# Kernel tuning notes

Hardware: AMD Instinct MI355X
Metric: run time of the kernel (lower is better)

Reference implementation:

```python
import jax, jax.numpy as jnp
import numpy as np

ALPHA = 0.2  # LeakyReLU negative slope
MASK_VAL = -9e15


def gat_layer(h, W, a, adj):
    # h: (b, n, f_in); W: (H, f_in, d); a: (H, 2d, 1); adj: (n, n)
    Wh = jnp.einsum('bni,hid->bhnd', h, W)          # (b, H, n, d)
    d = W.shape[-1]
    a1 = a[:, :d, 0]                                # (H, d) -> source term
    a2 = a[:, d:, 0]                                # (H, d) -> target term
    f1 = jnp.einsum('bhnd,hd->bhn', Wh, a1)
    f2 = jnp.einsum('bhnd,hd->bhn', Wh, a2)
    e = jax.nn.leaky_relu(f1[..., :, None] + f2[..., None, :], ALPHA)  # (b, H, n, n)
    e = jnp.where(adj > 0, e, MASK_VAL)
    att = jax.nn.softmax(e, axis=-1)
    out = jnp.einsum('bhij,bhjd->bhid', att, Wh)    # (b, H, n, d)
    b, H, n, dd = out.shape
    # concat heads along feature dim (matches torch.cat(head_outputs, dim=2))
    return jnp.transpose(out, (0, 2, 1, 3)).reshape(b, n, H * dd)


def setup_inputs() -> dict:
    key = jax.random.key(0)
    ks = jax.random.split(key, 8)
    B, N = 131072, 9
    HID, OUT, HEADS = 96, 48, 3
    hd1 = HID // HEADS   # 32
    hd2 = OUT // HEADS   # 16

    def xavier(k, shape, gain=1.414):
        fan_in, fan_out = shape[-2], shape[-1]
        lim = gain * np.sqrt(6.0 / (fan_in + fan_out))
        return jax.random.uniform(k, shape, jnp.float32, -lim, lim)

    obs = jax.random.normal(ks[0], (B, N), dtype=jnp.float32)
    adj = jnp.ones((N, N), dtype=jnp.float32)
    W1 = xavier(ks[1], (HEADS, 1, hd1))
    a1 = xavier(ks[2], (HEADS, 2 * hd1, 1))
    W2 = xavier(ks[3], (HEADS, HID, hd2))
    a2 = xavier(ks[4], (HEADS, 2 * hd2, 1))
    lim = np.sqrt(1.0 / OUT)
    Wp1 = jax.random.uniform(ks[5], (OUT, OUT // 2), jnp.float32, -lim, lim)
    bp1 = jnp.zeros((OUT // 2,), jnp.float32)
    lim2 = np.sqrt(1.0 / (OUT // 2))
    Wp2 = jax.random.uniform(ks[6], (OUT // 2, 1), jnp.float32, -lim2, lim2)
    bp2 = jnp.zeros((1,), jnp.float32)
    return {"obs": obs, "adj": adj, "W1": W1, "a1": a1, "W2": W2, "a2": a2,
            "Wp1": Wp1, "bp1": bp1, "Wp2": Wp2, "bp2": bp2}


def reference(obs, adj, W1, a1, W2, a2, Wp1, bp1, Wp2, bp2):
    h = obs[..., None]                       # (b, n, 1)
    h = jax.nn.elu(gat_layer(h, W1, a1, adj))
    h = gat_layer(h, W2, a2, adj)            # (b, n, output_dim)
    # attention pooling over nodes
    scores = jnp.tanh(h @ Wp1 + bp1) @ Wp2 + bp2   # (b, n, 1)
    w = jax.nn.softmax(scores, axis=1)
    return jnp.sum(w * h, axis=1)            # (b, output_dim)
```

## Files before the change

### kernel.cpp

```cpp
#include <hip/hip_runtime.h>
#include <math.h>

typedef _Float16 h16;
typedef _Float16 v2h __attribute__((ext_vector_type(2)));

#define ALPHA 0.2f
#define MASKV -9000000000000000.0f

constexpr int GSCR = 268;
constexpr int O_S  = 0;
constexpr int O_F1 = 28;
constexpr int O_F2 = 56;
constexpr int O_U  = 92;

#if defined(__has_builtin)
#  if __has_builtin(__builtin_amdgcn_fdot2)
#    define FDOT2(a,b,c) __builtin_amdgcn_fdot2((a),(b),(c),false)
#  endif
#endif
#ifndef FDOT2
__device__ __forceinline__ float fdot2_sw(v2h a, v2h b, float c) {
    return c + (float)a.x*(float)b.x + (float)a.y*(float)b.y;
}
#  define FDOT2(a,b,c) fdot2_sw((a),(b),(c))
#endif

union U4 { float4 f; v2h h[4]; };
union U2 { float2 f; v2h h[2]; };
union U1 { float  f; v2h h;    };

#define WAVE_SYNC() asm volatile("s_waitcnt lgkmcnt(0)" ::: "memory")

__device__ __forceinline__ float fast_rcp(float x) { return __builtin_amdgcn_rcpf(x); }
__device__ __forceinline__ float tanh_fast(float x) {
    float e = __expf(x + x);
    return 1.f - 2.f * fast_rcp(e + 1.f);
}

__global__ void prep_kernel(const float* __restrict__ W2, const float* __restrict__ Wp1,
                            h16* __restrict__ ws) {
    int t = blockIdx.x * 256 + threadIdx.x;
    if (t < 48 * 96) {
        int c = t / 96, i = t - c * 96;
        int h = c >> 4, d = c & 15;
        ws[t] = (h16)W2[(h * 96 + i) * 16 + d];
    } else if (t < 48 * 96 + 576) {
        int t2 = t - 48 * 96;
        int k = t2 / 24, s = t2 - k * 24;
        int l = s / 3, kp = s - 3 * l;
        int clo = l + 16 * kp, chi = clo + 8;
        ws[4608 + 2 * t2]     = (h16)Wp1[clo * 24 + k];
        ws[4608 + 2 * t2 + 1] = (h16)Wp1[chi * 24 + k];
    }
}

__global__ __launch_bounds__(128, 4) void gnn_gat_kernel(
    const float* __restrict__ obs, const float* __restrict__ adj,
    const float* __restrict__ W1,  const float* __restrict__ a1,
    const float* __restrict__ a2,  const float* __restrict__ bp1,
    const float* __restrict__ Wp2, const h16* __restrict__ ws,
    float* __restrict__ out, int B)
{
    __shared__ float sW1[96];
    __shared__ float sAdj[81];
    __shared__ float sC12[6];
    __shared__ __align__(16) float smem[16 * GSCR];

    const int tid = threadIdx.x;
    if (tid < 96) sW1[tid] = W1[tid];
    if (tid < 81) sAdj[tid] = adj[tid];
    if (tid < 6) {
        int gg = tid >> 1, w = tid & 1;
        float s = 0.f;
        for (int d = 0; d < 32; ++d)
            s += W1[gg * 32 + d] * a1[gg * 64 + w * 32 + d];
        sC12[tid] = s;
    }
    __syncthreads();

    const int wv = tid >> 6, lane = tid & 63;
    const int q = lane >> 3, l8 = lane & 7;
    float* g = smem + (wv * 8 + q) * GSCR;
    float4* hUf4 = (float4*)(g + O_U);
    float4* h2f4 = (float4*)g;
    const float4* wsf4 = (const float4*)ws;

    float c12[6];
    #pragma unroll
    for (int i = 0; i < 6; ++i) c12[i] = sC12[i];
    float a2a0[3], a2a1[3], a2b0[3], a2b1[3];
    #pragma unroll
    for (int h = 0; h < 3; ++h) {
        a2a0[h] = a2[h * 32 + l8];
        a2a1[h] = a2[h * 32 + 8 + l8];
        a2b0[h] = a2[h * 32 + 16 + l8];
        a2b1[h] = a2[h * 32 + 24 + l8];
    }
    unsigned am[3];
    #pragma unroll
    for (int r = 0; r < 3; ++r) {
        unsigned u = 0;
        for (int t = 0; t < 27; ++t)
            u |= (sAdj[r * 27 + t] > 0.f ? 1u : 0u) << t;
        am[r] = u;
    }
    float wq[3], bq[3];
    #pragma unroll
    for (int kk = 0; kk < 3; ++kk) {
        wq[kk] = Wp2[l8 + 8 * kk];
        bq[kk] = bp1[l8 + 8 * kk];
    }

    const int slots = gridDim.x * 16;
    for (int b = (blockIdx.x * 2 + wv) * 8 + q; b < B; b += slots) {
        float o_r[9];
        #pragma unroll
        for (int j = 0; j < 9; ++j) o_r[j] = obs[(size_t)b * 9 + j];

        for (int t = l8; t < 27; t += 8) {
            int gg = (t >= 18) ? 2 : (t >= 9 ? 1 : 0);
            int n = t - 9 * gg;
            float f1 = c12[2 * gg] * o_r[n];
            float c2 = c12[2 * gg + 1];
            unsigned rbits = (am[n / 3] >> (9 * (n % 3))) & 0x1FFu;
            float e[9], m = -3.0e38f;
            #pragma unroll
            for (int j = 0; j < 9; ++j) {
                float x = f1 + c2 * o_r[j];
                x = x > 0.f ? x : ALPHA * x;
                x = ((rbits >> j) & 1) ? x : MASKV;
                e[j] = x; m = fmaxf(m, x);
            }
            float sum = 0.f, sw = 0.f;
            #pragma unroll
            for (int j = 0; j < 9; ++j) {
                float p = __expf(e[j] - m);
                sum += p; sw += p * o_r[j];
            }
            g[O_S + t] = sw * fast_rcp(sum);
        }
        WAVE_SYNC();

        float acc[9][6];
        #pragma unroll
        for (int n = 0; n < 9; ++n)
            #pragma unroll
            for (int k = 0; k < 6; ++k) acc[n][k] = 0.f;

        for (int p = 0; p < 3; ++p) {
            #pragma unroll
            for (int it = 0; it < 5; ++it) {
                int t = l8 + 8 * it;
                if (t < 36) {
                    int n = t >> 2, ib = t & 3;
                    int i0 = 32 * p + 8 * ib;
                    float sv = g[O_S + p * 9 + n];
                    float4 wa = *(const float4*)&sW1[i0];
                    float4 wb = *(const float4*)&sW1[i0 + 4];
                    float v0 = sv * wa.x, v1 = sv * wa.y, v2 = sv * wa.z, v3 = sv * wa.w;
                    float v4 = sv * wb.x, v5 = sv * wb.y, v6 = sv * wb.z, v7 = sv * wb.w;
                    v0 = v0 > 0.f ? v0 : __expf(v0) - 1.f;
                    v1 = v1 > 0.f ? v1 : __expf(v1) - 1.f;
                    v2 = v2 > 0.f ? v2 : __expf(v2) - 1.f;
                    v3 = v3 > 0.f ? v3 : __expf(v3) - 1.f;
                    v4 = v4 > 0.f ? v4 : __expf(v4) - 1.f;
                    v5 = v5 > 0.f ? v5 : __expf(v5) - 1.f;
                    v6 = v6 > 0.f ? v6 : __expf(v6) - 1.f;
                    v7 = v7 > 0.f ? v7 : __expf(v7) - 1.f;
                    U4 u;
                    u.h[0] = (v2h){(h16)v0, (h16)v1};
                    u.h[1] = (v2h){(h16)v2, (h16)v3};
                    u.h[2] = (v2h){(h16)v4, (h16)v5};
                    u.h[3] = (v2h){(h16)v6, (h16)v7};
                    hUf4[n * 4 + ib] = u.f;
                }
            }
            WAVE_SYNC();

            #pragma unroll
            for (int ib = 0; ib < 4; ++ib) {
                U4 w[6];
                #pragma unroll
                for (int k = 0; k < 6; ++k)
                    w[k].f = wsf4[(l8 + 8 * k) * 12 + p * 4 + ib];
                #pragma unroll
                for (int n = 0; n < 9; ++n) {
                    U4 hh; hh.f = hUf4[n * 4 + ib];
                    #pragma unroll
                    for (int k = 0; k < 6; ++k) {
                        float a = acc[n][k];
                        a = FDOT2(hh.h[0], w[k].h[0], a);
                        a = FDOT2(hh.h[1], w[k].h[1], a);
                        a = FDOT2(hh.h[2], w[k].h[2], a);
                        a = FDOT2(hh.h[3], w[k].h[3], a);
                        acc[n][k] = a;
                    }
                }
            }
            WAVE_SYNC();
        }

        #pragma unroll
        for (int h = 0; h < 3; ++h) {
            #pragma unroll
            for (int n = 0; n < 9; ++n) {
                float v1 = acc[n][2 * h] * a2a0[h] + acc[n][2 * h + 1] * a2a1[h];
                float v2 = acc[n][2 * h] * a2b0[h] + acc[n][2 * h + 1] * a2b1[h];
                v1 += __shfl_xor(v1, 1, 8); v1 += __shfl_xor(v1, 2, 8); v1 += __shfl_xor(v1, 4, 8);
                v2 += __shfl_xor(v2, 1, 8); v2 += __shfl_xor(v2, 2, 8); v2 += __shfl_xor(v2, 4, 8);
                if (((h * 9 + n) & 7) == l8) {
                    g[O_F1 + h * 9 + n]  = v1;
                    g[O_F2 + h * 10 + n] = v2;
                }
            }
        }
        WAVE_SYNC();

        for (int t = l8; t < 27; t += 8) {
            int h = (t >= 18) ? 2 : (t >= 9 ? 1 : 0);
            int i = t - 9 * h;
            float f1i = g[O_F1 + t];
            float f2r[9];
            #pragma unroll
            for (int j = 0; j < 9; ++j) f2r[j] = g[O_F2 + h * 10 + j];
            unsigned rbits = (am[i / 3] >> (9 * (i % 3))) & 0x1FFu;
            float e[9], m = -3.0e38f;
            #pragma unroll
            for (int j = 0; j < 9; ++j) {
                float x = f1i + f2r[j];
                x = x > 0.f ? x : ALPHA * x;
                x = ((rbits >> j) & 1) ? x : MASKV;
                e[j] = x; m = fmaxf(m, x);
            }
            float p[9], sum = 0.f;
            #pragma unroll
            for (int j = 0; j < 9; ++j) { p[j] = __expf(e[j] - m); sum += p[j]; }
            float r = fast_rcp(sum);
            char* row = (char*)(g + O_U) + t * 24;
            U2 u01, u23; U1 u4;
            u01.h[0] = (v2h){(h16)(p[0] * r), (h16)(p[1] * r)};
            u01.h[1] = (v2h){(h16)(p[2] * r), (h16)(p[3] * r)};
            u23.h[0] = (v2h){(h16)(p[4] * r), (h16)(p[5] * r)};
            u23.h[1] = (v2h){(h16)(p[6] * r), (h16)(p[7] * r)};
            u4.h     = (v2h){(h16)(p[8] * r), (h16)0.f};
            *(float2*)(row)      = u01.f;
            *(float2*)(row + 8)  = u23.f;
            *(float*)(row + 16)  = u4.f;
        }
        WAVE_SYNC();

        #pragma unroll
        for (int h = 0; h < 3; ++h) {
            float t0[9], t1[9];
            #pragma unroll
            for (int i = 0; i < 9; ++i) {
                const char* row = (const char*)(g + O_U) + (h * 9 + i) * 24;
                U2 a01, a23; U1 a4;
                a01.f = *(const float2*)row;
                a23.f = *(const float2*)(row + 8);
                a4.f  = *(const float*)(row + 16);
                float pj[9];
                pj[0] = (float)a01.h[0].x; pj[1] = (float)a01.h[0].y;
                pj[2] = (float)a01.h[1].x; pj[3] = (float)a01.h[1].y;
                pj[4] = (float)a23.h[0].x; pj[5] = (float)a23.h[0].y;
                pj[6] = (float)a23.h[1].x; pj[7] = (float)a23.h[1].y;
                pj[8] = (float)a4.h.x;
                float s0 = 0.f, s1 = 0.f;
                #pragma unroll
                for (int j = 0; j < 9; ++j) {
                    s0 += pj[j] * acc[j][2 * h];
                    s1 += pj[j] * acc[j][2 * h + 1];
                }
                t0[i] = s0; t1[i] = s1;
            }
            #pragma unroll
            for (int i = 0; i < 9; ++i) { acc[i][2 * h] = t0[i]; acc[i][2 * h + 1] = t1[i]; }
        }

        #pragma unroll
        for (int n = 0; n < 9; ++n) {
            #pragma unroll
            for (int kp = 0; kp < 3; ++kp) {
                U1 u; u.h = (v2h){(h16)acc[n][2 * kp], (h16)acc[n][2 * kp + 1]};
                ((float*)g)[n * 24 + 3 * l8 + kp] = u.f;
            }
        }
        WAVE_SYNC();

        float sp[9];
        #pragma unroll
        for (int n = 0; n < 9; ++n) sp[n] = 0.f;
        #pragma unroll
        for (int kk = 0; kk < 3; ++kk) {
            int k = l8 + 8 * kk;
            U4 w0, w1, w2u, w3, w4, w5;
            w0.f = wsf4[576 + k * 6 + 0];
            w1.f = wsf4[576 + k * 6 + 1];
            w2u.f = wsf4[576 + k * 6 + 2];
            w3.f = wsf4[576 + k * 6 + 3];
            w4.f = wsf4[576 + k * 6 + 4];
            w5.f = wsf4[576 + k * 6 + 5];
            #pragma unroll
            for (int n = 0; n < 9; ++n) {
                float a = 0.f;
                U4 x;
                x.f = h2f4[n * 6 + 0];
                a = FDOT2(x.h[0], w0.h[0], a); a = FDOT2(x.h[1], w0.h[1], a);
                a = FDOT2(x.h[2], w0.h[2], a); a = FDOT2(x.h[3], w0.h[3], a);
                x.f = h2f4[n * 6 + 1];
                a = FDOT2(x.h[0], w1.h[0], a); a = FDOT2(x.h[1], w1.h[1], a);
                a = FDOT2(x.h[2], w1.h[2], a); a = FDOT2(x.h[3], w1.h[3], a);
                x.f = h2f4[n * 6 + 2];
                a = FDOT2(x.h[0], w2u.h[0], a); a = FDOT2(x.h[1], w2u.h[1], a);
                a = FDOT2(x.h[2], w2u.h[2], a); a = FDOT2(x.h[3], w2u.h[3], a);
                x.f = h2f4[n * 6 + 3];
                a = FDOT2(x.h[0], w3.h[0], a); a = FDOT2(x.h[1], w3.h[1], a);
                a = FDOT2(x.h[2], w3.h[2], a); a = FDOT2(x.h[3], w3.h[3], a);
                x.f = h2f4[n * 6 + 4];
                a = FDOT2(x.h[0], w4.h[0], a); a = FDOT2(x.h[1], w4.h[1], a);
                a = FDOT2(x.h[2], w4.h[2], a); a = FDOT2(x.h[3], w4.h[3], a);
                x.f = h2f4[n * 6 + 5];
                a = FDOT2(x.h[0], w5.h[0], a); a = FDOT2(x.h[1], w5.h[1], a);
                a = FDOT2(x.h[2], w5.h[2], a); a = FDOT2(x.h[3], w5.h[3], a);
                float tv = tanh_fast(a + bq[kk]);
                sp[n] += tv * wq[kk];
            }
        }
        #pragma unroll
        for (int n = 0; n < 9; ++n) {
            sp[n] += __shfl_xor(sp[n], 1, 8);
            sp[n] += __shfl_xor(sp[n], 2, 8);
            sp[n] += __shfl_xor(sp[n], 4, 8);
        }

        float mx = sp[0];
        #pragma unroll
        for (int n = 1; n < 9; ++n) mx = fmaxf(mx, sp[n]);
        float wn9[9], sum = 0.f;
        #pragma unroll
        for (int n = 0; n < 9; ++n) { wn9[n] = __expf(sp[n] - mx); sum += wn9[n]; }
        float r = fast_rcp(sum);
        #pragma unroll
        for (int k = 0; k < 6; ++k) {
            float ov = 0.f;
            #pragma unroll
            for (int n = 0; n < 9; ++n) ov += wn9[n] * acc[n][k];
            out[(size_t)b * 48 + l8 + 8 * k] = ov * r;
        }
        WAVE_SYNC();
    }
}

extern "C" void kernel_launch(void* const* d_in, const int* in_sizes, int n_in,
                              void* d_out, int out_size, void* d_ws, size_t ws_size,
                              hipStream_t stream) {
    const float* obs = (const float*)d_in[0];
    const float* adj = (const float*)d_in[1];
    const float* W1  = (const float*)d_in[2];
    const float* a1  = (const float*)d_in[3];
    const float* W2  = (const float*)d_in[4];
    const float* a2  = (const float*)d_in[5];
    const float* Wp1 = (const float*)d_in[6];
    const float* bp1 = (const float*)d_in[7];
    const float* Wp2 = (const float*)d_in[8];
    float* out = (float*)d_out;
    h16* ws = (h16*)d_ws;

    const int B = in_sizes[0] / 9;

    prep_kernel<<<(48 * 96 + 576 + 255) / 256, 256, 0, stream>>>(W2, Wp1, ws);

    gnn_gat_kernel<<<4096, 128, 0, stream>>>(
        obs, adj, W1, a1, a2, bp1, Wp2, ws, out, B);
}
```

Measured before the change: 363.0 us.

## Assign 16 lanes per batch element instead of 8 to cut per-thread work

Each batch element is now processed by a 16-lane group instead of an 8-lane group, so each lane holds 3 output columns instead of 6. This halves accumulator registers, which can raise occupancy and shorten per-thread serial work. Work is re-split across all stages: attention, the W2 matmul, the projection with 24 of 32 lanes active, and the shuffle reductions, which gain an extra step. A block of 128 threads now covers 8 elements instead of 16 with the same grid, so each block does more loop iterations and some lanes sit idle in several phases.

```diff
diff --git a/kernel.cpp b/kernel.cpp
--- a/kernel.cpp
+++ b/kernel.cpp
@@ -44,13 +44,10 @@
         int c = t / 96, i = t - c * 96;
         int h = c >> 4, d = c & 15;
         ws[t] = (h16)W2[(h * 96 + i) * 16 + d];
-    } else if (t < 48 * 96 + 576) {
+    } else if (t < 48 * 96 + 24 * 48) {
         int t2 = t - 48 * 96;
-        int k = t2 / 24, s = t2 - k * 24;
-        int l = s / 3, kp = s - 3 * l;
-        int clo = l + 16 * kp, chi = clo + 8;
-        ws[4608 + 2 * t2]     = (h16)Wp1[clo * 24 + k];
-        ws[4608 + 2 * t2 + 1] = (h16)Wp1[chi * 24 + k];
+        int k = t2 / 48, c = t2 - k * 48;
+        ws[4608 + t2] = (h16)Wp1[c * 24 + k];
     }
 }
 
@@ -64,7 +61,7 @@
     __shared__ float sW1[96];
     __shared__ float sAdj[81];
     __shared__ float sC12[6];
-    __shared__ __align__(16) float smem[16 * GSCR];
+    __shared__ __align__(16) float smem[8 * GSCR];
 
     const int tid = threadIdx.x;
     if (tid < 96) sW1[tid] = W1[tid];
@@ -78,24 +75,14 @@
     }
     __syncthreads();
 
-    const int wv = tid >> 6, lane = tid & 63;
-    const int q = lane >> 3, l8 = lane & 7;
-    float* g = smem + (wv * 8 + q) * GSCR;
+    const int gid = tid >> 4;
+    const int l16 = tid & 15;
+    float* g = smem + gid * GSCR;
     float4* hUf4 = (float4*)(g + O_U);
     float4* h2f4 = (float4*)g;
+    h16*   h2h   = (h16*)g;
     const float4* wsf4 = (const float4*)ws;
 
-    float c12[6];
-    #pragma unroll
-    for (int i = 0; i < 6; ++i) c12[i] = sC12[i];
-    float a2a0[3], a2a1[3], a2b0[3], a2b1[3];
-    #pragma unroll
-    for (int h = 0; h < 3; ++h) {
-        a2a0[h] = a2[h * 32 + l8];
-        a2a1[h] = a2[h * 32 + 8 + l8];
-        a2b0[h] = a2[h * 32 + 16 + l8];
-        a2b1[h] = a2[h * 32 + 24 + l8];
-    }
     unsigned am[3];
     #pragma unroll
     for (int r = 0; r < 3; ++r) {
@@ -104,53 +91,51 @@
             u |= (sAdj[r * 27 + t] > 0.f ? 1u : 0u) << t;
         am[r] = u;
     }
-    float wq[3], bq[3];
-    #pragma unroll
-    for (int kk = 0; kk < 3; ++kk) {
-        wq[kk] = Wp2[l8 + 8 * kk];
-        bq[kk] = bp1[l8 + 8 * kk];
-    }
-
-    const int slots = gridDim.x * 16;
-    for (int b = (blockIdx.x * 2 + wv) * 8 + q; b < B; b += slots) {
+
+    const int slots = gridDim.x * 8;
+    for (int b = blockIdx.x * 8 + gid; b < B; b += slots) {
         float o_r[9];
         #pragma unroll
         for (int j = 0; j < 9; ++j) o_r[j] = obs[(size_t)b * 9 + j];
 
-        for (int t = l8; t < 27; t += 8) {
-            int gg = (t >= 18) ? 2 : (t >= 9 ? 1 : 0);
-            int n = t - 9 * gg;
-            float f1 = c12[2 * gg] * o_r[n];
-            float c2 = c12[2 * gg + 1];
-            unsigned rbits = (am[n / 3] >> (9 * (n % 3))) & 0x1FFu;
-            float e[9], m = -3.0e38f;
-            #pragma unroll
-            for (int j = 0; j < 9; ++j) {
-                float x = f1 + c2 * o_r[j];
-                x = x > 0.f ? x : ALPHA * x;
-                x = ((rbits >> j) & 1) ? x : MASKV;
-                e[j] = x; m = fmaxf(m, x);
-            }
-            float sum = 0.f, sw = 0.f;
-            #pragma unroll
-            for (int j = 0; j < 9; ++j) {
-                float p = __expf(e[j] - m);
-                sum += p; sw += p * o_r[j];
-            }
-            g[O_S + t] = sw * fast_rcp(sum);
-        }
-        WAVE_SYNC();
-
-        float acc[9][6];
+        #pragma unroll
+        for (int it = 0; it < 2; ++it) {
+            int t = l16 + 16 * it;
+            if (t < 27) {
+                int gg = (t >= 18) ? 2 : (t >= 9 ? 1 : 0);
+                int n = t - 9 * gg;
+                float f1 = sC12[2 * gg] * o_r[n];
+                float c2 = sC12[2 * gg + 1];
+                unsigned rbits = (am[n / 3] >> (9 * (n % 3))) & 0x1FFu;
+                float e[9], m = -3.0e38f;
+                #pragma unroll
+                for (int j = 0; j < 9; ++j) {
+                    float x = f1 + c2 * o_r[j];
+                    x = x > 0.f ? x : ALPHA * x;
+                    x = ((rbits >> j) & 1) ? x : MASKV;
+                    e[j] = x; m = fmaxf(m, x);
+                }
+                float sum = 0.f, sw = 0.f;
+                #pragma unroll
+                for (int j = 0; j < 9; ++j) {
+                    float p = __expf(e[j] - m);
+                    sum += p; sw += p * o_r[j];
+                }
+                g[O_S + t] = sw * fast_rcp(sum);
+            }
+        }
+        WAVE_SYNC();
+
+        float acc[9][3];
         #pragma unroll
         for (int n = 0; n < 9; ++n)
             #pragma unroll
-            for (int k = 0; k < 6; ++k) acc[n][k] = 0.f;
+            for (int kk = 0; kk < 3; ++kk) acc[n][kk] = 0.f;
 
         for (int p = 0; p < 3; ++p) {
             #pragma unroll
-            for (int it = 0; it < 5; ++it) {
-                int t = l8 + 8 * it;
+            for (int it = 0; it < 3; ++it) {
+                int t = l16 + 16 * it;
                 if (t < 36) {
                     int n = t >> 2, ib = t & 3;
                     int i0 = 32 * p + 8 * ib;
@@ -179,21 +164,21 @@
 
             #pragma unroll
             for (int ib = 0; ib < 4; ++ib) {
-                U4 w[6];
-                #pragma unroll
-                for (int k = 0; k < 6; ++k)
-                    w[k].f = wsf4[(l8 + 8 * k) * 12 + p * 4 + ib];
+                U4 w[3];
+                #pragma unroll
+                for (int kk = 0; kk < 3; ++kk)
+                    w[kk].f = wsf4[(l16 + 16 * kk) * 12 + p * 4 + ib];
                 #pragma unroll
                 for (int n = 0; n < 9; ++n) {
                     U4 hh; hh.f = hUf4[n * 4 + ib];
                     #pragma unroll
-                    for (int k = 0; k < 6; ++k) {
-                        float a = acc[n][k];
-                        a = FDOT2(hh.h[0], w[k].h[0], a);
-                        a = FDOT2(hh.h[1], w[k].h[1], a);
-                        a = FDOT2(hh.h[2], w[k].h[2], a);
-                        a = FDOT2(hh.h[3], w[k].h[3], a);
-                        acc[n][k] = a;
+                    for (int kk = 0; kk < 3; ++kk) {
+                        float a = acc[n][kk];
+                        a = FDOT2(hh.h[0], w[kk].h[0], a);
+                        a = FDOT2(hh.h[1], w[kk].h[1], a);
+                        a = FDOT2(hh.h[2], w[kk].h[2], a);
+                        a = FDOT2(hh.h[3], w[kk].h[3], a);
+                        acc[n][kk] = a;
                     }
                 }
             }
@@ -202,13 +187,17 @@
 
         #pragma unroll
         for (int h = 0; h < 3; ++h) {
+            float aa = a2[h * 32 + l16];
+            float ab = a2[h * 32 + 16 + l16];
             #pragma unroll
             for (int n = 0; n < 9; ++n) {
-                float v1 = acc[n][2 * h] * a2a0[h] + acc[n][2 * h + 1] * a2a1[h];
-                float v2 = acc[n][2 * h] * a2b0[h] + acc[n][2 * h + 1] * a2b1[h];
-                v1 += __shfl_xor(v1, 1, 8); v1 += __shfl_xor(v1, 2, 8); v1 += __shfl_xor(v1, 4, 8);
-                v2 += __shfl_xor(v2, 1, 8); v2 += __shfl_xor(v2, 2, 8); v2 += __shfl_xor(v2, 4, 8);
-                if (((h * 9 + n) & 7) == l8) {
+                float v1 = acc[n][h] * aa;
+                float v2 = acc[n][h] * ab;
+                v1 += __shfl_xor(v1, 1, 16); v1 += __shfl_xor(v1, 2, 16);
+                v1 += __shfl_xor(v1, 4, 16); v1 += __shfl_xor(v1, 8, 16);
+                v2 += __shfl_xor(v2, 1, 16); v2 += __shfl_xor(v2, 2, 16);
+                v2 += __shfl_xor(v2, 4, 16); v2 += __shfl_xor(v2, 8, 16);
+                if (((h * 9 + n) & 15) == l16) {
                     g[O_F1 + h * 9 + n]  = v1;
                     g[O_F2 + h * 10 + n] = v2;
                 }
@@ -216,42 +205,46 @@
         }
         WAVE_SYNC();
 
-        for (int t = l8; t < 27; t += 8) {
-            int h = (t >= 18) ? 2 : (t >= 9 ? 1 : 0);
-            int i = t - 9 * h;
-            float f1i = g[O_F1 + t];
-            float f2r[9];
-            #pragma unroll
-            for (int j = 0; j < 9; ++j) f2r[j] = g[O_F2 + h * 10 + j];
-            unsigned rbits = (am[i / 3] >> (9 * (i % 3))) & 0x1FFu;
-            float e[9], m = -3.0e38f;
-            #pragma unroll
-            for (int j = 0; j < 9; ++j) {
-                float x = f1i + f2r[j];
-                x = x > 0.f ? x : ALPHA * x;
-                x = ((rbits >> j) & 1) ? x : MASKV;
-                e[j] = x; m = fmaxf(m, x);
-            }
-            float p[9], sum = 0.f;
-            #pragma unroll
-            for (int j = 0; j < 9; ++j) { p[j] = __expf(e[j] - m); sum += p[j]; }
-            float r = fast_rcp(sum);
-            char* row = (char*)(g + O_U) + t * 24;
-            U2 u01, u23; U1 u4;
-            u01.h[0] = (v2h){(h16)(p[0] * r), (h16)(p[1] * r)};
-            u01.h[1] = (v2h){(h16)(p[2] * r), (h16)(p[3] * r)};
-            u23.h[0] = (v2h){(h16)(p[4] * r), (h16)(p[5] * r)};
-            u23.h[1] = (v2h){(h16)(p[6] * r), (h16)(p[7] * r)};
-            u4.h     = (v2h){(h16)(p[8] * r), (h16)0.f};
-            *(float2*)(row)      = u01.f;
-            *(float2*)(row + 8)  = u23.f;
-            *(float*)(row + 16)  = u4.f;
+        #pragma unroll
+        for (int it = 0; it < 2; ++it) {
+            int t = l16 + 16 * it;
+            if (t < 27) {
+                int h = (t >= 18) ? 2 : (t >= 9 ? 1 : 0);
+                int i = t - 9 * h;
+                float f1i = g[O_F1 + t];
+                float f2r[9];
+                #pragma unroll
+                for (int j = 0; j < 9; ++j) f2r[j] = g[O_F2 + h * 10 + j];
+                unsigned rbits = (am[i / 3] >> (9 * (i % 3))) & 0x1FFu;
+                float e[9], m = -3.0e38f;
+                #pragma unroll
+                for (int j = 0; j < 9; ++j) {
+                    float x = f1i + f2r[j];
+                    x = x > 0.f ? x : ALPHA * x;
+                    x = ((rbits >> j) & 1) ? x : MASKV;
+                    e[j] = x; m = fmaxf(m, x);
+                }
+                float p[9], sum = 0.f;
+                #pragma unroll
+                for (int j = 0; j < 9; ++j) { p[j] = __expf(e[j] - m); sum += p[j]; }
+                float r = fast_rcp(sum);
+                char* row = (char*)(g + O_U) + t * 24;
+                U2 u01, u23; U1 u4;
+                u01.h[0] = (v2h){(h16)(p[0] * r), (h16)(p[1] * r)};
+                u01.h[1] = (v2h){(h16)(p[2] * r), (h16)(p[3] * r)};
+                u23.h[0] = (v2h){(h16)(p[4] * r), (h16)(p[5] * r)};
+                u23.h[1] = (v2h){(h16)(p[6] * r), (h16)(p[7] * r)};
+                u4.h     = (v2h){(h16)(p[8] * r), (h16)0.f};
+                *(float2*)(row)      = u01.f;
+                *(float2*)(row + 8)  = u23.f;
+                *(float*)(row + 16)  = u4.f;
+            }
         }
         WAVE_SYNC();
 
         #pragma unroll
         for (int h = 0; h < 3; ++h) {
-            float t0[9], t1[9];
+            float tv[9];
             #pragma unroll
             for (int i = 0; i < 9; ++i) {
                 const char* row = (const char*)(g + O_U) + (h * 9 + i) * 24;
@@ -265,25 +258,20 @@
                 pj[4] = (float)a23.h[0].x; pj[5] = (float)a23.h[0].y;
                 pj[6] = (float)a23.h[1].x; pj[7] = (float)a23.h[1].y;
                 pj[8] = (float)a4.h.x;
-                float s0 = 0.f, s1 = 0.f;
-                #pragma unroll
-                for (int j = 0; j < 9; ++j) {
-                    s0 += pj[j] * acc[j][2 * h];
-                    s1 += pj[j] * acc[j][2 * h + 1];
-                }
-                t0[i] = s0; t1[i] = s1;
-            }
-            #pragma unroll
-            for (int i = 0; i < 9; ++i) { acc[i][2 * h] = t0[i]; acc[i][2 * h + 1] = t1[i]; }
+                float s = 0.f;
+                #pragma unroll
+                for (int j = 0; j < 9; ++j) s += pj[j] * acc[j][h];
+                tv[i] = s;
+            }
+            #pragma unroll
+            for (int i = 0; i < 9; ++i) acc[i][h] = tv[i];
         }
 
         #pragma unroll
         for (int n = 0; n < 9; ++n) {
             #pragma unroll
-            for (int kp = 0; kp < 3; ++kp) {
-                U1 u; u.h = (v2h){(h16)acc[n][2 * kp], (h16)acc[n][2 * kp + 1]};
-                ((float*)g)[n * 24 + 3 * l8 + kp] = u.f;
-            }
+            for (int kk = 0; kk < 3; ++kk)
+                h2h[n * 48 + l16 + 16 * kk] = (h16)acc[n][kk];
         }
         WAVE_SYNC();
 
@@ -291,46 +279,39 @@
         #pragma unroll
         for (int n = 0; n < 9; ++n) sp[n] = 0.f;
         #pragma unroll
-        for (int kk = 0; kk < 3; ++kk) {
-            int k = l8 + 8 * kk;
-            U4 w0, w1, w2u, w3, w4, w5;
-            w0.f = wsf4[576 + k * 6 + 0];
-            w1.f = wsf4[576 + k * 6 + 1];
-            w2u.f = wsf4[576 + k * 6 + 2];
-            w3.f = wsf4[576 + k * 6 + 3];
-            w4.f = wsf4[576 + k * 6 + 4];
-            w5.f = wsf4[576 + k * 6 + 5];
-            #pragma unroll
-            for (int n = 0; n < 9; ++n) {
-                float a = 0.f;
-                U4 x;
-                x.f = h2f4[n * 6 + 0];
-                a = FDOT2(x.h[0], w0.h[0], a); a = FDOT2(x.h[1], w0.h[1], a);
-                a = FDOT2(x.h[2], w0.h[2], a); a = FDOT2(x.h[3], w0.h[3], a);
-                x.f = h2f4[n * 6 + 1];
-                a = FDOT2(x.h[0], w1.h[0], a); a = FDOT2(x.h[1], w1.h[1], a);
-                a = FDOT2(x.h[2], w1.h[2], a); a = FDOT2(x.h[3], w1.h[3], a);
-                x.f = h2f4[n * 6 + 2];
-                a = FDOT2(x.h[0], w2u.h[0], a); a = FDOT2(x.h[1], w2u.h[1], a);
-                a = FDOT2(x.h[2], w2u.h[2], a); a = FDOT2(x.h[3], w2u.h[3], a);
-                x.f = h2f4[n * 6 + 3];
-                a = FDOT2(x.h[0], w3.h[0], a); a = FDOT2(x.h[1], w3.h[1], a);
-                a = FDOT2(x.h[2], w3.h[2], a); a = FDOT2(x.h[3], w3.h[3], a);
-                x.f = h2f4[n * 6 + 4];
-                a = FDOT2(x.h[0], w4.h[0], a); a = FDOT2(x.h[1], w4.h[1], a);
-                a = FDOT2(x.h[2], w4.h[2], a); a = FDOT2(x.h[3], w4.h[3], a);
-                x.f = h2f4[n * 6 + 5];
-                a = FDOT2(x.h[0], w5.h[0], a); a = FDOT2(x.h[1], w5.h[1], a);
-                a = FDOT2(x.h[2], w5.h[2], a); a = FDOT2(x.h[3], w5.h[3], a);
-                float tv = tanh_fast(a + bq[kk]);
-                sp[n] += tv * wq[kk];
-            }
+        for (int kk = 0; kk < 2; ++kk) {
+            int k = l16 + 16 * kk;
+            const bool valid = (k < 24);
+            const int k2 = valid ? k : 0;
+            float wqv = valid ? Wp2[k] : 0.f;
+            float bqv = valid ? bp1[k] : 0.f;
+            float a9[9];
+            #pragma unroll
+            for (int n = 0; n < 9; ++n) a9[n] = 0.f;
+            #pragma unroll
+            for (int j = 0; j < 6; ++j) {
+                U4 w; w.f = wsf4[576 + k2 * 6 + j];
+                #pragma unroll
+                for (int n = 0; n < 9; ++n) {
+                    U4 x; x.f = h2f4[n * 6 + j];
+                    float a = a9[n];
+                    a = FDOT2(x.h[0], w.h[0], a);
+                    a = FDOT2(x.h[1], w.h[1], a);
+                    a = FDOT2(x.h[2], w.h[2], a);
+                    a = FDOT2(x.h[3], w.h[3], a);
+                    a9[n] = a;
+                }
+            }
+            #pragma unroll
+            for (int n = 0; n < 9; ++n)
+                sp[n] += tanh_fast(a9[n] + bqv) * wqv;
         }
         #pragma unroll
         for (int n = 0; n < 9; ++n) {
-            sp[n] += __shfl_xor(sp[n], 1, 8);
-            sp[n] += __shfl_xor(sp[n], 2, 8);
-            sp[n] += __shfl_xor(sp[n], 4, 8);
+            sp[n] += __shfl_xor(sp[n], 1, 16);
+            sp[n] += __shfl_xor(sp[n], 2, 16);
+            sp[n] += __shfl_xor(sp[n], 4, 16);
+            sp[n] += __shfl_xor(sp[n], 8, 16);
         }
 
         float mx = sp[0];
@@ -341,11 +322,11 @@
         for (int n = 0; n < 9; ++n) { wn9[n] = __expf(sp[n] - mx); sum += wn9[n]; }
         float r = fast_rcp(sum);
         #pragma unroll
-        for (int k = 0; k < 6; ++k) {
+        for (int kk = 0; kk < 3; ++kk) {
             float ov = 0.f;
             #pragma unroll
-            for (int n = 0; n < 9; ++n) ov += wn9[n] * acc[n][k];
-            out[(size_t)b * 48 + l8 + 8 * k] = ov * r;
+            for (int n = 0; n < 9; ++n) ov += wn9[n] * acc[n][kk];
+            out[(size_t)b * 48 + l16 + 16 * kk] = ov * r;
         }
         WAVE_SYNC();
     }
@@ -368,7 +349,7 @@
 
     const int B = in_sizes[0] / 9;
 
-    prep_kernel<<<(48 * 96 + 576 + 255) / 256, 256, 0, stream>>>(W2, Wp1, ws);
+    prep_kernel<<<(48 * 96 + 24 * 48 + 255) / 256, 256, 0, stream>>>(W2, Wp1, ws);
 
     gnn_gat_kernel<<<4096, 128, 0, stream>>>(
         obs, adj, W1, a1, a2, bp1, Wp2, ws, out, B);
```

New measurement: 982.5 us. 2.71x slower.
